# Optimization experiments

Hardware: AMD Instinct MI355X
Metric: run time of the kernel (lower is better)

## Reference

```python
import jax, jax.numpy as jnp
import numpy as np

N_HEAD = 8
N_QP = 4  # query/key points per head
N_VP = 4  # value points per head
D_SPH = 16  # scalar dims per head
SCALE_SCALAR = D_SPH ** (-0.5)
SCALE_POINT = (4.5 * N_QP) ** (-0.5)
SCALE_TOTAL = 3.0 ** (-0.5)  # scalar + pair bias + point logits


def _euclid(xp, r, t):
    # xp: (b,n,l,p,3), r: (b,l,3,3), t: (b,l,3)  -> row-vector convention: x @ r + t
    return jnp.einsum('bnlpk,blkc->bnlpc', xp, r) + t[:, None, :, None, :]


def _inv_euclid(xp, r, t):
    # (x - t) @ r^T
    return jnp.einsum('bnlpk,blck->bnlpc', xp - t[:, None, :, None, :], r)


def setup_inputs() -> dict:
    key = jax.random.key(0)
    ks = jax.random.split(key, 16)
    b, l, d_res, d_pair = 2, 512, 384, 128
    w = lambda k, shp, fan: jax.random.normal(k, shp, jnp.float32) * (fan ** -0.5)
    return {
        'x': jax.random.normal(ks[0], (b, l, d_res), jnp.float32),
        'e': jax.random.normal(ks[1], (b, l, l, d_pair), jnp.float32),
        'r': jax.random.normal(ks[2], (b, l, 3, 3), jnp.float32),
        't': jax.random.normal(ks[3], (b, l, 3), jnp.float32),
        'Wq_s': w(ks[4], (d_res, N_HEAD * D_SPH), d_res),
        'Wk_s': w(ks[5], (d_res, N_HEAD * D_SPH), d_res),
        'Wv_s': w(ks[6], (d_res, N_HEAD * D_SPH), d_res),
        'Wpb': w(ks[7], (d_pair, N_HEAD), d_pair),
        'Wq_p': w(ks[8], (d_res, N_HEAD * N_QP * 3), d_res),
        'Wk_p': w(ks[9], (d_res, N_HEAD * N_QP * 3), d_res),
        'Wv_p': w(ks[10], (d_res, N_HEAD * N_VP * 3), d_res),
        'gamma': jnp.log(jnp.expm1(jnp.ones((N_HEAD,), jnp.float32))),
        'Wout': w(ks[11], (N_HEAD * D_SPH + N_HEAD * d_pair + N_HEAD * N_VP * 3 + N_HEAD * N_VP, d_res), 1280),
        'bout': jnp.zeros((d_res,), jnp.float32),
    }


def reference(x, e, r, t, Wq_s, Wk_s, Wv_s, Wpb, Wq_p, Wk_p, Wv_p, gamma, Wout, bout):
    b, l, _ = x.shape
    n = N_HEAD

    def split_heads(v):  # (b,l,n*d) -> (b,n,l,d)
        return v.reshape(b, l, n, -1).transpose(0, 2, 1, 3)

    def split_points(v, p):  # (b,l,n*p*3) -> (b,n,l,p,3)
        return v.reshape(b, l, n, p, 3).transpose(0, 2, 1, 3, 4)

    q_s, k_s, v_s = (split_heads(x @ W) for W in (Wq_s, Wk_s, Wv_s))
    q_p = _euclid(split_points(x @ Wq_p, N_QP), r, t)
    k_p = _euclid(split_points(x @ Wk_p, N_QP), r, t)
    v_p = _euclid(split_points(x @ Wv_p, N_VP), r, t)

    logit_scalar = jnp.einsum('bnid,bnjd->bnij', q_s, k_s) * SCALE_SCALAR
    bias_pair = (e @ Wpb).transpose(0, 3, 1, 2)  # (b,n,i,j)
    # pairwise squared point distances, summed over points p and coords c
    diff = q_p[:, :, :, None] - k_p[:, :, None]  # (b,n,i,j,p,3)
    sqdist = (diff ** 2).sum(axis=(-1, -2))      # (b,n,i,j)
    logit_point = -0.5 * SCALE_POINT * gamma[None, :, None, None] * sqdist

    attn = jax.nn.softmax(SCALE_TOTAL * (logit_scalar + bias_pair + logit_point), axis=-1)

    out_scalar = jnp.einsum('bnij,bnjd->bnid', attn, v_s).transpose(0, 2, 1, 3).reshape(b, l, -1)
    out_pair = jnp.einsum('bnij,bijd->bnid', attn, e).transpose(0, 2, 1, 3).reshape(b, l, -1)
    out_point = jnp.einsum('bnij,bnjpc->bnipc', attn, v_p)
    out_point = _inv_euclid(out_point, r, t)  # (b,n,i,p,3)
    out_point_norm = jnp.sqrt((out_point ** 2).sum(-1))  # (b,n,i,p)
    out_point = out_point.transpose(0, 2, 1, 3, 4).reshape(b, l, -1)
    out_point_norm = out_point_norm.transpose(0, 2, 1, 3).reshape(b, l, -1)

    out = jnp.concatenate([out_scalar, out_pair, out_point, out_point_norm], axis=-1)
    return out @ Wout + bout
```

## Files before the change

### kernel.cpp

```cpp
#include <hip/hip_runtime.h>
#include <hip/hip_bf16.h>
#include <math.h>

#define NH 8
#define L 512
#define DP 128
#define DS 16
#define DCAT 1280
#define TJ 32
#define NCHUNK 4
#define CJ 128
#define PSTRIDE 1280

#define SCALE_SCALAR 0.25f
#define SCALE_POINT  0.23570226039551584f
#define SCALE_TOTAL  0.5773502691896258f

typedef __bf16 bf16_t;
typedef bf16_t bf16x8 __attribute__((ext_vector_type(8)));
typedef float  f32x4v __attribute__((ext_vector_type(4)));

__global__ __launch_bounds__(256) void k_pack(
    const float* __restrict__ x,
    const float* __restrict__ Wq_s, const float* __restrict__ Wk_s, const float* __restrict__ Wv_s,
    const float* __restrict__ Wq_p, const float* __restrict__ Wk_p, const float* __restrict__ Wv_p,
    __hip_bfloat16* __restrict__ xb, __hip_bfloat16* __restrict__ WallT) {
    int idx = blockIdx.x * 256 + threadIdx.x;
    const int T1 = 1024 * 384;
    if (idx < T1) {
        xb[idx] = __float2bfloat16(x[idx]);
    } else {
        int j = idx - T1;
        int n = j / 384, k = j % 384;
        float v;
        if      (n < 128) v = Wq_s[k * 128 + n];
        else if (n < 256) v = Wk_s[k * 128 + (n - 128)];
        else if (n < 384) v = Wv_s[k * 128 + (n - 256)];
        else if (n < 480) v = Wq_p[k * 96  + (n - 384)];
        else if (n < 576) v = Wk_p[k * 96  + (n - 480)];
        else              v = Wv_p[k * 96  + (n - 576)];
        WallT[(size_t)n * 384 + k] = __float2bfloat16(v);
    }
}

__global__ __launch_bounds__(256) void k_prep(const float* __restrict__ Wout,
                                              __hip_bfloat16* __restrict__ WoutT) {
    __shared__ float tile[64][65];
    const int tid = threadIdx.x;
    const int k0 = blockIdx.x * 64;
    const int n0 = blockIdx.y * 64;
#pragma unroll
    for (int s = 0; s < 16; ++s) {
        int idx = s * 256 + tid, kk = idx >> 6, nn = idx & 63;
        tile[kk][nn] = Wout[(size_t)(k0 + kk) * 384 + n0 + nn];
    }
    __syncthreads();
#pragma unroll
    for (int s = 0; s < 16; ++s) {
        int idx = s * 256 + tid, nn = idx >> 6, kk = idx & 63;
        WoutT[(size_t)(n0 + nn) * 1280 + k0 + kk] = __float2bfloat16(tile[kk][nn]);
    }
}

__global__ __launch_bounds__(256) void k_projm(
    const __hip_bfloat16* __restrict__ xb, const __hip_bfloat16* __restrict__ WallT,
    float* __restrict__ q_s, float* __restrict__ k_s, float* __restrict__ v_s,
    float* __restrict__ praw) {
    __shared__ __align__(16) bf16_t As[64 * 40];
    __shared__ __align__(16) bf16_t Bs[48 * 40];
    const int tid = threadIdx.x;
    const int row0 = blockIdx.x * 64, col0 = blockIdx.y * 48;
    const int w = tid >> 6, lane = tid & 63;
    f32x4v acc[3] = {};

    for (int k0 = 0; k0 < 384; k0 += 32) {
        __syncthreads();
        {
            int rr = tid >> 2, q = tid & 3;
            *reinterpret_cast<int4*>(&As[rr * 40 + q * 8]) =
                *reinterpret_cast<const int4*>(&xb[(size_t)(row0 + rr) * 384 + k0 + q * 8]);
            if (tid < 192)
                *reinterpret_cast<int4*>(&Bs[rr * 40 + q * 8]) =
                    *reinterpret_cast<const int4*>(&WallT[(size_t)(col0 + rr) * 384 + k0 + q * 8]);
        }
        __syncthreads();
        const int m = lane & 15, kq = lane >> 4;
        bf16x8 af = *reinterpret_cast<const bf16x8*>(&As[(w * 16 + m) * 40 + kq * 8]);
#pragma unroll
        for (int c = 0; c < 3; ++c) {
            bf16x8 bfr = *reinterpret_cast<const bf16x8*>(&Bs[(c * 16 + m) * 40 + kq * 8]);
            acc[c] = __builtin_amdgcn_mfma_f32_16x16x32_bf16(af, bfr, acc[c], 0, 0, 0);
        }
    }
    const int colL = lane & 15, rbase = (lane >> 4) * 4;
#pragma unroll
    for (int c = 0; c < 3; ++c) {
        int col = col0 + c * 16 + colL;
#pragma unroll
        for (int rg = 0; rg < 4; ++rg) {
            int row = row0 + w * 16 + rbase + rg;
            float v = acc[c][rg];
            int bb = row >> 9, ll = row & 511;
            if (col < 384) {
                int kind = col >> 7, n = (col >> 4) & 7, d = col & 15;
                float* dst = (kind == 0) ? q_s : (kind == 1) ? k_s : v_s;
                dst[((size_t)(bb * NH + n) * L + ll) * DS + d] = v;
            } else {
                praw[(size_t)row * 288 + (col - 384)] = v;
            }
        }
    }
}

__global__ __launch_bounds__(256) void k_euclid(
    const float* __restrict__ praw, const float* __restrict__ r, const float* __restrict__ t,
    float* __restrict__ q_p, float* __restrict__ k_p, float* __restrict__ v_p) {
    int idx = blockIdx.x * 256 + threadIdx.x;
    int row = idx / 288, o = idx % 288;
    int arr = o / 96, oo = o % 96;
    int n = oo / 12, pc = oo % 12, p = pc / 3, c = pc % 3;
    const float* base = praw + (size_t)row * 288 + arr * 96 + n * 12 + p * 3;
    float acc = t[row * 3 + c];
#pragma unroll
    for (int k = 0; k < 3; ++k) acc += base[k] * r[row * 9 + k * 3 + c];
    float* dst = (arr == 0) ? q_p : (arr == 1) ? k_p : v_p;
    int bb = row >> 9, ll = row & 511;
    dst[((size_t)(bb * NH + n) * L + ll) * 12 + pc] = acc;
}

__global__ __launch_bounds__(256) void k_attn(
    const float* __restrict__ e, const float* __restrict__ Wpb, const float* __restrict__ gamma,
    const float* __restrict__ q_s, const float* __restrict__ k_s, const float* __restrict__ v_s,
    const float* __restrict__ q_p, const float* __restrict__ k_p, const float* __restrict__ v_p,
    float* __restrict__ part) {
    __shared__ __align__(16) float et[TJ * DP];
    __shared__ __align__(16) float wpbT[NH * DP];
    __shared__ float pt[NH][36];
    __shared__ float ptT[TJ][NH];
    __shared__ __align__(16) float qsl[NH * 16];
    __shared__ __align__(16) float qpl[NH * 12];
    __shared__ float gsh[NH];

    const int tid = threadIdx.x;
    const int blk = blockIdx.x;
    const int bi = blk >> 2, chunk = blk & 3;
    const int b = bi >> 9, i = bi & 511, b8 = b * NH;
    const int nH = tid >> 5, jL = tid & 31;
    const int d4 = tid & 31, jsub = tid >> 5;

    for (int idx = tid; idx < NH * DP; idx += 256)
        wpbT[(idx >> 7) * DP + (idx & 127)] = Wpb[(idx & 127) * NH + (idx >> 7)];
    if (tid < 128) {
        int n = tid >> 4, d = tid & 15;
        qsl[n * 16 + d] = q_s[((size_t)(b8 + n) * L + i) * DS + d];
    } else if (tid < 224) {
        int o = tid - 128, n = o / 12, pc = o % 12;
        qpl[n * 12 + pc] = q_p[((size_t)(b8 + n) * L + i) * 12 + pc];
    } else if (tid < 232) {
        gsh[tid - 224] = gamma[tid - 224];
    }

    const int nS = tid >> 4, dS = tid & 15;
    const int oP = tid - 128;
    const int nP = (oP >= 0 && oP < 96) ? oP / 12 : 0;
    const int pcP = (oP >= 0 && oP < 96) ? oP % 12 : 0;
    const float* vsp = v_s + (((size_t)(b8 + nS) * L + chunk * CJ) << 4) + dS;
    const float* vpp = v_p + ((size_t)(b8 + nP) * L + chunk * CJ) * 12 + pcP;

    float lsum = 0.f;
    float4 accPair[NH];
#pragma unroll
    for (int n = 0; n < NH; ++n) accPair[n] = make_float4(0.f, 0.f, 0.f, 0.f);
    float accS = 0.f, accP = 0.f;

    const float4* esrc4 = reinterpret_cast<const float4*>(
        e + ((size_t)(b * L + i) * L + chunk * CJ) * DP);

    for (int tile = 0; tile < CJ / TJ; ++tile) {
        const int j0 = tile * TJ;
        __syncthreads();
#pragma unroll
        for (int s = 0; s < 4; ++s) {
            int idx = tid + s * 256;
            int j = idx >> 5, g = idx & 31;
            float4 v = esrc4[(size_t)(j0 + j) * 32 + g];
            reinterpret_cast<float4*>(et)[j * 32 + (g ^ j)] = v;
        }
        __syncthreads();
        {
            const int jg = chunk * CJ + j0 + jL;
            const float4* row4 = reinterpret_cast<const float4*>(et) + jL * 32;
            const float4* wr4 = reinterpret_cast<const float4*>(&wpbT[nH * DP]);
            float bsum = 0.f;
#pragma unroll 8
            for (int g = 0; g < 32; ++g) {
                float4 ev = row4[g ^ jL];
                float4 wv4 = wr4[g];
                bsum += ev.x * wv4.x + ev.y * wv4.y + ev.z * wv4.z + ev.w * wv4.w;
            }
            const float4* ksr = reinterpret_cast<const float4*>(k_s + (((size_t)(b8 + nH) * L + jg) << 4));
            const float4* q4 = reinterpret_cast<const float4*>(&qsl[nH * 16]);
            float ssum = 0.f;
#pragma unroll
            for (int g = 0; g < 4; ++g) {
                float4 kv = ksr[g], qv = q4[g];
                ssum += kv.x * qv.x + kv.y * qv.y + kv.z * qv.z + kv.w * qv.w;
            }
            const float4* kpr = reinterpret_cast<const float4*>(k_p + ((size_t)(b8 + nH) * L + jg) * 12);
            const float4* qp4 = reinterpret_cast<const float4*>(&qpl[nH * 12]);
            float sq = 0.f;
#pragma unroll
            for (int g = 0; g < 3; ++g) {
                float4 kv = kpr[g], qv = qp4[g];
                float d0;
                d0 = qv.x - kv.x; sq += d0 * d0;  d0 = qv.y - kv.y; sq += d0 * d0;
                d0 = qv.z - kv.z; sq += d0 * d0;  d0 = qv.w - kv.w; sq += d0 * d0;
            }
            float lg = SCALE_TOTAL * (ssum * SCALE_SCALAR + bsum
                                      - 0.5f * SCALE_POINT * gsh[nH] * sq);
            float pv = __expf(lg);
            lsum += pv;
            pt[nH][jL] = pv;
            ptT[jL][nH] = pv;
        }
        __syncthreads();
        {
            const float4* et4 = reinterpret_cast<const float4*>(et);
#pragma unroll
            for (int s = 0; s < 4; ++s) {
                int j = jsub * 4 + s;
                float4 ev = et4[j * 32 + (d4 ^ j)];
                const float4* pb4 = reinterpret_cast<const float4*>(&ptT[j][0]);
                float4 pA = pb4[0], pB = pb4[1];
#define ACCP(nn, ps) accPair[nn].x += (ps) * ev.x; accPair[nn].y += (ps) * ev.y; \
                     accPair[nn].z += (ps) * ev.z; accPair[nn].w += (ps) * ev.w;
                ACCP(0, pA.x) ACCP(1, pA.y) ACCP(2, pA.z) ACCP(3, pA.w)
                ACCP(4, pB.x) ACCP(5, pB.y) ACCP(6, pB.z) ACCP(7, pB.w)
#undef ACCP
            }
        }
        if (tid < 128) {
            const float* vp = vsp + (size_t)j0 * 16;
#pragma unroll
            for (int q = 0; q < 8; ++q) {
                float4 p4 = *reinterpret_cast<const float4*>(&pt[nS][q * 4]);
                accS += p4.x * vp[(q * 4 + 0) * 16] + p4.y * vp[(q * 4 + 1) * 16]
                      + p4.z * vp[(q * 4 + 2) * 16] + p4.w * vp[(q * 4 + 3) * 16];
            }
        } else if (tid < 224) {
            const float* vp = vpp + (size_t)j0 * 12;
#pragma unroll
            for (int q = 0; q < 8; ++q) {
                float4 p4 = *reinterpret_cast<const float4*>(&pt[nP][q * 4]);
                accP += p4.x * vp[(q * 4 + 0) * 12] + p4.y * vp[(q * 4 + 1) * 12]
                      + p4.z * vp[(q * 4 + 2) * 12] + p4.w * vp[(q * 4 + 3) * 12];
            }
        }
    }

    float* prow = part + (size_t)blk * PSTRIDE;
    lsum += __shfl_xor(lsum, 1);  lsum += __shfl_xor(lsum, 2);
    lsum += __shfl_xor(lsum, 4);  lsum += __shfl_xor(lsum, 8);
    lsum += __shfl_xor(lsum, 16);
    if (jL == 0) prow[1248 + nH] = lsum;
    if (tid < 128) prow[1024 + tid] = accS;
    else if (tid < 224) prow[1152 + (tid - 128)] = accP;

    float4* red4 = reinterpret_cast<float4*>(et);
    __syncthreads();
    if (jsub >= 4) {
#pragma unroll
        for (int n = 0; n < NH; ++n) red4[((jsub - 4) * NH + n) * 32 + d4] = accPair[n];
    }
    __syncthreads();
    if (jsub < 4) {
#pragma unroll
        for (int n = 0; n < NH; ++n) {
            float4 o = red4[(jsub * NH + n) * 32 + d4];
            accPair[n].x += o.x; accPair[n].y += o.y; accPair[n].z += o.z; accPair[n].w += o.w;
        }
    }
    __syncthreads();
    if (jsub == 2 || jsub == 3) {
#pragma unroll
        for (int n = 0; n < NH; ++n) red4[((jsub - 2) * NH + n) * 32 + d4] = accPair[n];
    }
    __syncthreads();
    if (jsub < 2) {
#pragma unroll
        for (int n = 0; n < NH; ++n) {
            float4 o = red4[(jsub * NH + n) * 32 + d4];
            accPair[n].x += o.x; accPair[n].y += o.y; accPair[n].z += o.z; accPair[n].w += o.w;
        }
    }
    __syncthreads();
    if (jsub == 1) {
#pragma unroll
        for (int n = 0; n < NH; ++n) red4[n * 32 + d4] = accPair[n];
    }
    __syncthreads();
    if (jsub == 0) {
#pragma unroll
        for (int n = 0; n < NH; ++n) {
            float4 o = red4[n * 32 + d4];
            accPair[n].x += o.x; accPair[n].y += o.y; accPair[n].z += o.z; accPair[n].w += o.w;
            *reinterpret_cast<float4*>(&prow[n * 128 + d4 * 4]) = accPair[n];
        }
    }
}

__global__ __launch_bounds__(256) void k_comb(
    const float* __restrict__ part, const float* __restrict__ r, const float* __restrict__ t,
    __hip_bfloat16* __restrict__ concat) {
    __shared__ float comb[1256];
    __shared__ float rtsh[12], osh[96], o2sh[96];
    const int tid = threadIdx.x;
    const int bi = blockIdx.x;
    const float* base = part + (size_t)bi * NCHUNK * PSTRIDE;
#pragma unroll
    for (int s = 0; s < 5; ++s) {
        int idx = tid + s * 256;
        if (idx < 1256)
            comb[idx] = base[idx] + base[PSTRIDE + idx] + base[2 * PSTRIDE + idx] + base[3 * PSTRIDE + idx];
    }
    if (tid >= 244 && tid < 256) {
        int c = tid - 244;
        rtsh[c] = (c < 9) ? r[bi * 9 + c] : t[bi * 3 + (c - 9)];
    }
    __syncthreads();
    __hip_bfloat16* crow = concat + (size_t)bi * DCAT;
    if (tid < 128) crow[tid] = __float2bfloat16(comb[1024 + tid] / comb[1248 + (tid >> 4)]);
    for (int idx = tid; idx < 1024; idx += 256)
        crow[128 + idx] = __float2bfloat16(comb[idx] / comb[1248 + (idx >> 7)]);
    if (tid >= 128 && tid < 224) {
        int o = tid - 128;
        osh[o] = comb[1152 + o] / comb[1248 + o / 12];
    }
    __syncthreads();
    if (tid < 96) {
        int n = tid / 12, pc = tid % 12, p = pc / 3, c = pc % 3;
        float oc = 0.f;
#pragma unroll
        for (int k = 0; k < 3; ++k)
            oc += (osh[n * 12 + p * 3 + k] - rtsh[9 + k]) * rtsh[c * 3 + k];
        crow[1152 + tid] = __float2bfloat16(oc);
        o2sh[tid] = oc;
    }
    __syncthreads();
    if (tid < 32) {
        int n = tid >> 2, p = tid & 3;
        float vx = o2sh[n * 12 + p * 3], vy = o2sh[n * 12 + p * 3 + 1], vz = o2sh[n * 12 + p * 3 + 2];
        crow[1248 + tid] = __float2bfloat16(sqrtf(vx * vx + vy * vy + vz * vz));
    }
}

__global__ __launch_bounds__(256) void k_out(const __hip_bfloat16* __restrict__ A,
                                             const __hip_bfloat16* __restrict__ Bt,
                                             const float* __restrict__ bout,
                                             float* __restrict__ out) {
    __shared__ __align__(16) bf16_t At[64 * 40];
    __shared__ __align__(16) bf16_t Bs[64 * 40];
    const int tid = threadIdx.x;
    const int row0 = blockIdx.x * 64, col0 = blockIdx.y * 64;
    const int wv = tid >> 6, lane = tid & 63;
    f32x4v acc[4] = {};

    for (int k0 = 0; k0 < 1280; k0 += 32) {
        __syncthreads();
        {
            int rr = tid >> 2, q = tid & 3;
            *reinterpret_cast<int4*>(&At[rr * 40 + q * 8]) =
                *reinterpret_cast<const int4*>(&A[(size_t)(row0 + rr) * 1280 + k0 + q * 8]);
            *reinterpret_cast<int4*>(&Bs[rr * 40 + q * 8]) =
                *reinterpret_cast<const int4*>(&Bt[(size_t)(col0 + rr) * 1280 + k0 + q * 8]);
        }
        __syncthreads();
        const int m = lane & 15, kq = lane >> 4;
        bf16x8 af = *reinterpret_cast<const bf16x8*>(&At[(wv * 16 + m) * 40 + kq * 8]);
#pragma unroll
        for (int nt = 0; nt < 4; ++nt) {
            bf16x8 bfr = *reinterpret_cast<const bf16x8*>(&Bs[(nt * 16 + m) * 40 + kq * 8]);
            acc[nt] = __builtin_amdgcn_mfma_f32_16x16x32_bf16(af, bfr, acc[nt], 0, 0, 0);
        }
    }
    const int col_l = lane & 15, rbase = (lane >> 4) * 4;
#pragma unroll
    for (int nt = 0; nt < 4; ++nt) {
        int col = col0 + nt * 16 + col_l;
        float bo = bout[col];
#pragma unroll
        for (int rg = 0; rg < 4; ++rg) {
            int rowg = row0 + wv * 16 + rbase + rg;
            out[(size_t)rowg * 384 + col] = acc[nt][rg] + bo;
        }
    }
}

extern "C" void kernel_launch(void* const* d_in, const int* in_sizes, int n_in,
                              void* d_out, int out_size, void* d_ws, size_t ws_size,
                              hipStream_t stream) {
    const float* x     = (const float*)d_in[0];
    const float* e     = (const float*)d_in[1];
    const float* r     = (const float*)d_in[2];
    const float* t     = (const float*)d_in[3];
    const float* Wq_s  = (const float*)d_in[4];
    const float* Wk_s  = (const float*)d_in[5];
    const float* Wv_s  = (const float*)d_in[6];
    const float* Wpb   = (const float*)d_in[7];
    const float* Wq_p  = (const float*)d_in[8];
    const float* Wk_p  = (const float*)d_in[9];
    const float* Wv_p  = (const float*)d_in[10];
    const float* gamma = (const float*)d_in[11];
    const float* Wout  = (const float*)d_in[12];
    const float* bout  = (const float*)d_in[13];

    float* ws   = (float*)d_ws;
    float* q_s  = ws + 0;
    float* k_s  = ws + 131072;
    float* v_s  = ws + 262144;
    float* q_p  = ws + 393216;
    float* k_p  = ws + 491520;
    float* v_p  = ws + 589824;
    float* praw = ws + 688128;
    __hip_bfloat16* xb     = (__hip_bfloat16*)((char*)d_ws + 3932160);
    __hip_bfloat16* WallT  = (__hip_bfloat16*)((char*)d_ws + 4718592);
    __hip_bfloat16* concat = (__hip_bfloat16*)((char*)d_ws + 5234688);
    __hip_bfloat16* WoutT  = (__hip_bfloat16*)((char*)d_ws + 7856128);
    float* part = (float*)((char*)d_ws + 8847360);
    float* out = (float*)d_out;

    hipLaunchKernelGGL(k_pack, dim3(2544), dim3(256), 0, stream,
                       x, Wq_s, Wk_s, Wv_s, Wq_p, Wk_p, Wv_p, xb, WallT);
    hipLaunchKernelGGL(k_prep, dim3(20, 6), dim3(256), 0, stream, Wout, WoutT);
    hipLaunchKernelGGL(k_projm, dim3(16, 14), dim3(256), 0, stream,
                       xb, WallT, q_s, k_s, v_s, praw);
    hipLaunchKernelGGL(k_euclid, dim3(1152), dim3(256), 0, stream,
                       praw, r, t, q_p, k_p, v_p);
    hipLaunchKernelGGL(k_attn, dim3(4096), dim3(256), 0, stream,
                       e, Wpb, gamma, q_s, k_s, v_s, q_p, k_p, v_p, part);
    hipLaunchKernelGGL(k_comb, dim3(1024), dim3(256), 0, stream,
                       part, r, t, concat);
    hipLaunchKernelGGL(k_out, dim3(16, 6), dim3(256), 0, stream, concat, WoutT, bout, out);
}
```

Before: 486.6 us.

## Double-buffer pair tiles via direct global-to-LDS loads and split pair-bias reduction

```diff
diff --git a/kernel.cpp b/kernel.cpp
--- a/kernel.cpp
+++ b/kernel.cpp
@@ -133,8 +133,9 @@
     const float* __restrict__ q_s, const float* __restrict__ k_s, const float* __restrict__ v_s,
     const float* __restrict__ q_p, const float* __restrict__ k_p, const float* __restrict__ v_p,
     float* __restrict__ part) {
-    __shared__ __align__(16) float et[TJ * DP];
-    __shared__ __align__(16) float wpbT[NH * DP];
+    __shared__ __align__(16) float et[2][TJ * DP];
+    __shared__ __align__(16) float wpbK[DP * NH];
+    __shared__ float ps[8 * TJ * NH];
     __shared__ float pt[NH][36];
     __shared__ float ptT[TJ][NH];
     __shared__ __align__(16) float qsl[NH * 16];
@@ -148,8 +149,7 @@
     const int nH = tid >> 5, jL = tid & 31;
     const int d4 = tid & 31, jsub = tid >> 5;
 
-    for (int idx = tid; idx < NH * DP; idx += 256)
-        wpbT[(idx >> 7) * DP + (idx & 127)] = Wpb[(idx & 127) * NH + (idx >> 7)];
+    reinterpret_cast<float4*>(wpbK)[tid] = reinterpret_cast<const float4*>(Wpb)[tid];
     if (tid < 128) {
         int n = tid >> 4, d = tid & 15;
         qsl[n * 16 + d] = q_s[((size_t)(b8 + n) * L + i) * DS + d];
@@ -167,40 +167,56 @@
     const float* vsp = v_s + (((size_t)(b8 + nS) * L + chunk * CJ) << 4) + dS;
     const float* vpp = v_p + ((size_t)(b8 + nP) * L + chunk * CJ) * 12 + pcP;
 
-    float lsum = 0.f;
-    float4 accPair[NH];
-#pragma unroll
-    for (int n = 0; n < NH; ++n) accPair[n] = make_float4(0.f, 0.f, 0.f, 0.f);
-    float accS = 0.f, accP = 0.f;
-
     const float4* esrc4 = reinterpret_cast<const float4*>(
         e + ((size_t)(b * L + i) * L + chunk * CJ) * DP);
 
+    const int wbase = tid & 192;
+    auto stage = [&](int buf, int j0) {
+        float* etb = &et[buf][0];
+#pragma unroll
+        for (int s = 0; s < 4; ++s) {
+            int idx = s * 256 + tid;
+            int j = idx >> 5, g = (idx & 31) ^ j;
+            const float* src = reinterpret_cast<const float*>(esrc4 + (size_t)(j0 + j) * 32 + g);
+            __builtin_amdgcn_global_load_lds(
+                (const __attribute__((address_space(1))) void*)src,
+                (__attribute__((address_space(3))) void*)(etb + (size_t)(s * 256 + wbase) * 4),
+                16, 0, 0);
+        }
+    };
+
+    float lsum = 0.f;
+    f32x4v accPair[NH] = {};
+    float accS = 0.f, accP = 0.f;
+
+    stage(0, 0);
+    __syncthreads();
+
+    int cur = 0;
     for (int tile = 0; tile < CJ / TJ; ++tile) {
         const int j0 = tile * TJ;
-        __syncthreads();
-#pragma unroll
-        for (int s = 0; s < 4; ++s) {
-            int idx = tid + s * 256;
-            int j = idx >> 5, g = idx & 31;
-            float4 v = esrc4[(size_t)(j0 + j) * 32 + g];
-            reinterpret_cast<float4*>(et)[j * 32 + (g ^ j)] = v;
-        }
-        __syncthreads();
-        {
-            const int jg = chunk * CJ + j0 + jL;
-            const float4* row4 = reinterpret_cast<const float4*>(et) + jL * 32;
-            const float4* wr4 = reinterpret_cast<const float4*>(&wpbT[nH * DP]);
-            float bsum = 0.f;
-#pragma unroll 8
-            for (int g = 0; g < 32; ++g) {
-                float4 ev = row4[g ^ jL];
-                float4 wv4 = wr4[g];
-                bsum += ev.x * wv4.x + ev.y * wv4.y + ev.z * wv4.z + ev.w * wv4.w;
-            }
+        if (tile < CJ / TJ - 1) stage(cur ^ 1, j0 + TJ);
+
+        const f32x4v* e4 = reinterpret_cast<const f32x4v*>(&et[cur][0]);
+
+        f32x4v a0 = {}, a1 = {};
+        {
+            const f32x4v* wp4 = reinterpret_cast<const f32x4v*>(wpbK);
+#pragma unroll
+            for (int f = 0; f < 4; ++f) {
+                f32x4v ev = e4[jL * 32 + ((nH * 4 + f) ^ jL)];
+                const f32x4v* wk = wp4 + (size_t)(nH * 16 + f * 4) * 2;
+                a0 += ev.x * wk[0]; a1 += ev.x * wk[1];
+                a0 += ev.y * wk[2]; a1 += ev.y * wk[3];
+                a0 += ev.z * wk[4]; a1 += ev.z * wk[5];
+                a0 += ev.w * wk[6]; a1 += ev.w * wk[7];
+            }
+        }
+        const int jg = chunk * CJ + j0 + jL;
+        float ssum = 0.f, sq = 0.f;
+        {
             const float4* ksr = reinterpret_cast<const float4*>(k_s + (((size_t)(b8 + nH) * L + jg) << 4));
             const float4* q4 = reinterpret_cast<const float4*>(&qsl[nH * 16]);
-            float ssum = 0.f;
 #pragma unroll
             for (int g = 0; g < 4; ++g) {
                 float4 kv = ksr[g], qv = q4[g];
@@ -208,7 +224,6 @@
             }
             const float4* kpr = reinterpret_cast<const float4*>(k_p + ((size_t)(b8 + nH) * L + jg) * 12);
             const float4* qp4 = reinterpret_cast<const float4*>(&qpl[nH * 12]);
-            float sq = 0.f;
 #pragma unroll
             for (int g = 0; g < 3; ++g) {
                 float4 kv = kpr[g], qv = qp4[g];
@@ -216,6 +231,21 @@
                 d0 = qv.x - kv.x; sq += d0 * d0;  d0 = qv.y - kv.y; sq += d0 * d0;
                 d0 = qv.z - kv.z; sq += d0 * d0;  d0 = qv.w - kv.w; sq += d0 * d0;
             }
+        }
+        {
+            int pb = (nH * TJ + jL) * NH, sw = jL & 7;
+            ps[pb + (0 ^ sw)] = a0.x; ps[pb + (1 ^ sw)] = a0.y;
+            ps[pb + (2 ^ sw)] = a0.z; ps[pb + (3 ^ sw)] = a0.w;
+            ps[pb + (4 ^ sw)] = a1.x; ps[pb + (5 ^ sw)] = a1.y;
+            ps[pb + (6 ^ sw)] = a1.z; ps[pb + (7 ^ sw)] = a1.w;
+        }
+        __syncthreads();
+
+        {
+            float bsum = 0.f;
+            const int sw = nH ^ (jL & 7);
+#pragma unroll
+            for (int kq = 0; kq < 8; ++kq) bsum += ps[(kq * TJ + jL) * NH + sw];
             float lg = SCALE_TOTAL * (ssum * SCALE_SCALAR + bsum
                                       - 0.5f * SCALE_POINT * gsh[nH] * sq);
             float pv = __expf(lg);
@@ -224,19 +254,18 @@
             ptT[jL][nH] = pv;
         }
         __syncthreads();
-        {
-            const float4* et4 = reinterpret_cast<const float4*>(et);
+
+        {
 #pragma unroll
             for (int s = 0; s < 4; ++s) {
                 int j = jsub * 4 + s;
-                float4 ev = et4[j * 32 + (d4 ^ j)];
+                f32x4v ev = e4[j * 32 + (d4 ^ j)];
                 const float4* pb4 = reinterpret_cast<const float4*>(&ptT[j][0]);
                 float4 pA = pb4[0], pB = pb4[1];
-#define ACCP(nn, ps) accPair[nn].x += (ps) * ev.x; accPair[nn].y += (ps) * ev.y; \
-                     accPair[nn].z += (ps) * ev.z; accPair[nn].w += (ps) * ev.w;
-                ACCP(0, pA.x) ACCP(1, pA.y) ACCP(2, pA.z) ACCP(3, pA.w)
-                ACCP(4, pB.x) ACCP(5, pB.y) ACCP(6, pB.z) ACCP(7, pB.w)
-#undef ACCP
+                accPair[0] += pA.x * ev; accPair[1] += pA.y * ev;
+                accPair[2] += pA.z * ev; accPair[3] += pA.w * ev;
+                accPair[4] += pB.x * ev; accPair[5] += pB.y * ev;
+                accPair[6] += pB.z * ev; accPair[7] += pB.w * ev;
             }
         }
         if (tid < 128) {
@@ -256,6 +285,8 @@
                       + p4.z * vp[(q * 4 + 2) * 12] + p4.w * vp[(q * 4 + 3) * 12];
             }
         }
+        __syncthreads();
+        cur ^= 1;
     }
 
     float* prow = part + (size_t)blk * PSTRIDE;
@@ -266,7 +297,7 @@
     if (tid < 128) prow[1024 + tid] = accS;
     else if (tid < 224) prow[1152 + (tid - 128)] = accP;
 
-    float4* red4 = reinterpret_cast<float4*>(et);
+    f32x4v* red4 = reinterpret_cast<f32x4v*>(&et[0][0]);
     __syncthreads();
     if (jsub >= 4) {
 #pragma unroll
@@ -275,36 +306,29 @@
     __syncthreads();
     if (jsub < 4) {
 #pragma unroll
+        for (int n = 0; n < NH; ++n) accPair[n] += red4[(jsub * NH + n) * 32 + d4];
+    }
+    __syncthreads();
+    if (jsub == 2 || jsub == 3) {
+#pragma unroll
+        for (int n = 0; n < NH; ++n) red4[((jsub - 2) * NH + n) * 32 + d4] = accPair[n];
+    }
+    __syncthreads();
+    if (jsub < 2) {
+#pragma unroll
+        for (int n = 0; n < NH; ++n) accPair[n] += red4[(jsub * NH + n) * 32 + d4];
+    }
+    __syncthreads();
+    if (jsub == 1) {
+#pragma unroll
+        for (int n = 0; n < NH; ++n) red4[n * 32 + d4] = accPair[n];
+    }
+    __syncthreads();
+    if (jsub == 0) {
+#pragma unroll
         for (int n = 0; n < NH; ++n) {
-            float4 o = red4[(jsub * NH + n) * 32 + d4];
-            accPair[n].x += o.x; accPair[n].y += o.y; accPair[n].z += o.z; accPair[n].w += o.w;
-        }
-    }
-    __syncthreads();
-    if (jsub == 2 || jsub == 3) {
-#pragma unroll
-        for (int n = 0; n < NH; ++n) red4[((jsub - 2) * NH + n) * 32 + d4] = accPair[n];
-    }
-    __syncthreads();
-    if (jsub < 2) {
-#pragma unroll
-        for (int n = 0; n < NH; ++n) {
-            float4 o = red4[(jsub * NH + n) * 32 + d4];
-            accPair[n].x += o.x; accPair[n].y += o.y; accPair[n].z += o.z; accPair[n].w += o.w;
-        }
-    }
-    __syncthreads();
-    if (jsub == 1) {
-#pragma unroll
-        for (int n = 0; n < NH; ++n) red4[n * 32 + d4] = accPair[n];
-    }
-    __syncthreads();
-    if (jsub == 0) {
-#pragma unroll
-        for (int n = 0; n < NH; ++n) {
-            float4 o = red4[n * 32 + d4];
-            accPair[n].x += o.x; accPair[n].y += o.y; accPair[n].z += o.z; accPair[n].w += o.w;
-            *reinterpret_cast<float4*>(&prow[n * 128 + d4 * 4]) = accPair[n];
+            accPair[n] += red4[n * 32 + d4];
+            *reinterpret_cast<f32x4v*>(&prow[n * 128 + d4 * 4]) = accPair[n];
         }
     }
 }
```

New measurement: 554.4 us. +13.9%, slower.

## Keep e tile in registers, pad LDS rows, remap bias threads to head-major

Applied to the files above, without the earlier changes.

```diff
diff --git a/kernel.cpp b/kernel.cpp
--- a/kernel.cpp
+++ b/kernel.cpp
@@ -133,23 +133,27 @@
     const float* __restrict__ q_s, const float* __restrict__ k_s, const float* __restrict__ v_s,
     const float* __restrict__ q_p, const float* __restrict__ k_p, const float* __restrict__ v_p,
     float* __restrict__ part) {
-    __shared__ __align__(16) float et[TJ * DP];
-    __shared__ __align__(16) float wpbT[NH * DP];
-    __shared__ float pt[NH][36];
-    __shared__ float ptT[TJ][NH];
+    __shared__ __align__(16) float et[TJ * 132];
+    __shared__ __align__(16) float wpbT[NH * 132];
+    __shared__ __align__(16) float pt[NH][36];
     __shared__ __align__(16) float qsl[NH * 16];
     __shared__ __align__(16) float qpl[NH * 12];
     __shared__ float gsh[NH];
+    __shared__ float lred[32];
 
     const int tid = threadIdx.x;
     const int blk = blockIdx.x;
     const int bi = blk >> 2, chunk = blk & 3;
     const int b = bi >> 9, i = bi & 511, b8 = b * NH;
-    const int nH = tid >> 5, jL = tid & 31;
-    const int d4 = tid & 31, jsub = tid >> 5;
-
-    for (int idx = tid; idx < NH * DP; idx += 256)
-        wpbT[(idx >> 7) * DP + (idx & 127)] = Wpb[(idx & 127) * NH + (idx >> 7)];
+
+    const int wA = tid >> 6, nA = (tid >> 3) & 7, jrA = tid & 7;
+    const int jA = wA * 8 + jrA;
+    const int jr2 = tid >> 5, g = tid & 31;
+
+    for (int idx = tid; idx < NH * DP; idx += 256) {
+        int n = idx >> 7, k = idx & 127;
+        wpbT[n * 132 + k] = Wpb[k * NH + n];
+    }
     if (tid < 128) {
         int n = tid >> 4, d = tid & 15;
         qsl[n * 16 + d] = q_s[((size_t)(b8 + n) * L + i) * DS + d];
@@ -167,76 +171,66 @@
     const float* vsp = v_s + (((size_t)(b8 + nS) * L + chunk * CJ) << 4) + dS;
     const float* vpp = v_p + ((size_t)(b8 + nP) * L + chunk * CJ) * 12 + pcP;
 
+    const f32x4v* esrc4 = reinterpret_cast<const f32x4v*>(
+        e + ((size_t)(b * L + i) * L + chunk * CJ) * DP);
+    f32x4v* et4 = reinterpret_cast<f32x4v*>(et);
+
     float lsum = 0.f;
-    float4 accPair[NH];
-#pragma unroll
-    for (int n = 0; n < NH; ++n) accPair[n] = make_float4(0.f, 0.f, 0.f, 0.f);
+    f32x4v accPair[NH] = {};
     float accS = 0.f, accP = 0.f;
-
-    const float4* esrc4 = reinterpret_cast<const float4*>(
-        e + ((size_t)(b * L + i) * L + chunk * CJ) * DP);
+    f32x4v ev[4];
 
     for (int tile = 0; tile < CJ / TJ; ++tile) {
         const int j0 = tile * TJ;
         __syncthreads();
 #pragma unroll
         for (int s = 0; s < 4; ++s) {
-            int idx = tid + s * 256;
-            int j = idx >> 5, g = idx & 31;
-            float4 v = esrc4[(size_t)(j0 + j) * 32 + g];
-            reinterpret_cast<float4*>(et)[j * 32 + (g ^ j)] = v;
+            int j = jr2 + 8 * s;
+            f32x4v v = esrc4[(size_t)(j0 + j) * 32 + g];
+            et4[j * 33 + g] = v;
+            ev[s] = v;
         }
         __syncthreads();
         {
-            const int jg = chunk * CJ + j0 + jL;
-            const float4* row4 = reinterpret_cast<const float4*>(et) + jL * 32;
-            const float4* wr4 = reinterpret_cast<const float4*>(&wpbT[nH * DP]);
-            float bsum = 0.f;
+            const f32x4v* erow = et4 + jA * 33;
+            const f32x4v* wrow = reinterpret_cast<const f32x4v*>(wpbT) + nA * 33;
+            f32x4v b4 = {};
 #pragma unroll 8
-            for (int g = 0; g < 32; ++g) {
-                float4 ev = row4[g ^ jL];
-                float4 wv4 = wr4[g];
-                bsum += ev.x * wv4.x + ev.y * wv4.y + ev.z * wv4.z + ev.w * wv4.w;
+            for (int gg = 0; gg < 32; ++gg) b4 += erow[gg] * wrow[gg];
+            float bsum = b4[0] + b4[1] + b4[2] + b4[3];
+
+            const int jg = chunk * CJ + j0 + jA;
+            const f32x4v* ksr = reinterpret_cast<const f32x4v*>(k_s + (((size_t)(b8 + nA) * L + jg) << 4));
+            const f32x4v* q4 = reinterpret_cast<const f32x4v*>(&qsl[nA * 16]);
+            f32x4v s4 = {};
+#pragma unroll
+            for (int gg = 0; gg < 4; ++gg) s4 += ksr[gg] * q4[gg];
+            float ssum = s4[0] + s4[1] + s4[2] + s4[3];
+
+            const f32x4v* kpr = reinterpret_cast<const f32x4v*>(k_p + ((size_t)(b8 + nA) * L + jg) * 12);
+            const f32x4v* qp4 = reinterpret_cast<const f32x4v*>(&qpl[nA * 12]);
+            f32x4v d4 = {};
+#pragma unroll
+            for (int gg = 0; gg < 3; ++gg) {
+                f32x4v df = qp4[gg] - kpr[gg];
+                d4 += df * df;
             }
-            const float4* ksr = reinterpret_cast<const float4*>(k_s + (((size_t)(b8 + nH) * L + jg) << 4));
-            const float4* q4 = reinterpret_cast<const float4*>(&qsl[nH * 16]);
-            float ssum = 0.f;
-#pragma unroll
-            for (int g = 0; g < 4; ++g) {
-                float4 kv = ksr[g], qv = q4[g];
-                ssum += kv.x * qv.x + kv.y * qv.y + kv.z * qv.z + kv.w * qv.w;
-            }
-            const float4* kpr = reinterpret_cast<const float4*>(k_p + ((size_t)(b8 + nH) * L + jg) * 12);
-            const float4* qp4 = reinterpret_cast<const float4*>(&qpl[nH * 12]);
-            float sq = 0.f;
-#pragma unroll
-            for (int g = 0; g < 3; ++g) {
-                float4 kv = kpr[g], qv = qp4[g];
-                float d0;
-                d0 = qv.x - kv.x; sq += d0 * d0;  d0 = qv.y - kv.y; sq += d0 * d0;
-                d0 = qv.z - kv.z; sq += d0 * d0;  d0 = qv.w - kv.w; sq += d0 * d0;
-            }
+            float sq = d4[0] + d4[1] + d4[2] + d4[3];
+
             float lg = SCALE_TOTAL * (ssum * SCALE_SCALAR + bsum
-                                      - 0.5f * SCALE_POINT * gsh[nH] * sq);
+                                      - 0.5f * SCALE_POINT * gsh[nA] * sq);
             float pv = __expf(lg);
             lsum += pv;
-            pt[nH][jL] = pv;
-            ptT[jL][nH] = pv;
+            pt[nA][jA] = pv;
         }
         __syncthreads();
         {
-            const float4* et4 = reinterpret_cast<const float4*>(et);
 #pragma unroll
             for (int s = 0; s < 4; ++s) {
-                int j = jsub * 4 + s;
-                float4 ev = et4[j * 32 + (d4 ^ j)];
-                const float4* pb4 = reinterpret_cast<const float4*>(&ptT[j][0]);
-                float4 pA = pb4[0], pB = pb4[1];
-#define ACCP(nn, ps) accPair[nn].x += (ps) * ev.x; accPair[nn].y += (ps) * ev.y; \
-                     accPair[nn].z += (ps) * ev.z; accPair[nn].w += (ps) * ev.w;
-                ACCP(0, pA.x) ACCP(1, pA.y) ACCP(2, pA.z) ACCP(3, pA.w)
-                ACCP(4, pB.x) ACCP(5, pB.y) ACCP(6, pB.z) ACCP(7, pB.w)
-#undef ACCP
+                int j = jr2 + 8 * s;
+#pragma unroll
+                for (int n = 0; n < NH; ++n)
+                    accPair[n] += pt[n][j] * ev[s];
             }
         }
         if (tid < 128) {
@@ -259,52 +253,45 @@
     }
 
     float* prow = part + (size_t)blk * PSTRIDE;
-    lsum += __shfl_xor(lsum, 1);  lsum += __shfl_xor(lsum, 2);
-    lsum += __shfl_xor(lsum, 4);  lsum += __shfl_xor(lsum, 8);
-    lsum += __shfl_xor(lsum, 16);
-    if (jL == 0) prow[1248 + nH] = lsum;
+    lsum += __shfl_xor(lsum, 1);  lsum += __shfl_xor(lsum, 2);  lsum += __shfl_xor(lsum, 4);
+    if (jrA == 0) lred[wA * 8 + nA] = lsum;
     if (tid < 128) prow[1024 + tid] = accS;
     else if (tid < 224) prow[1152 + (tid - 128)] = accP;
-
-    float4* red4 = reinterpret_cast<float4*>(et);
-    __syncthreads();
+    __syncthreads();
+    if (tid < 8) prow[1248 + tid] = lred[tid] + lred[8 + tid] + lred[16 + tid] + lred[24 + tid];
+
+    f32x4v* red4 = reinterpret_cast<f32x4v*>(et);
+    const int d4i = tid & 31, jsub = tid >> 5;
     if (jsub >= 4) {
 #pragma unroll
-        for (int n = 0; n < NH; ++n) red4[((jsub - 4) * NH + n) * 32 + d4] = accPair[n];
+        for (int n = 0; n < NH; ++n) red4[((jsub - 4) * NH + n) * 32 + d4i] = accPair[n];
     }
     __syncthreads();
     if (jsub < 4) {
 #pragma unroll
+        for (int n = 0; n < NH; ++n) accPair[n] += red4[(jsub * NH + n) * 32 + d4i];
+    }
+    __syncthreads();
+    if (jsub == 2 || jsub == 3) {
+#pragma unroll
+        for (int n = 0; n < NH; ++n) red4[((jsub - 2) * NH + n) * 32 + d4i] = accPair[n];
+    }
+    __syncthreads();
+    if (jsub < 2) {
+#pragma unroll
+        for (int n = 0; n < NH; ++n) accPair[n] += red4[(jsub * NH + n) * 32 + d4i];
+    }
+    __syncthreads();
+    if (jsub == 1) {
+#pragma unroll
+        for (int n = 0; n < NH; ++n) red4[n * 32 + d4i] = accPair[n];
+    }
+    __syncthreads();
+    if (jsub == 0) {
+#pragma unroll
         for (int n = 0; n < NH; ++n) {
-            float4 o = red4[(jsub * NH + n) * 32 + d4];
-            accPair[n].x += o.x; accPair[n].y += o.y; accPair[n].z += o.z; accPair[n].w += o.w;
-        }
-    }
-    __syncthreads();
-    if (jsub == 2 || jsub == 3) {
-#pragma unroll
-        for (int n = 0; n < NH; ++n) red4[((jsub - 2) * NH + n) * 32 + d4] = accPair[n];
-    }
-    __syncthreads();
-    if (jsub < 2) {
-#pragma unroll
-        for (int n = 0; n < NH; ++n) {
-            float4 o = red4[(jsub * NH + n) * 32 + d4];
-            accPair[n].x += o.x; accPair[n].y += o.y; accPair[n].z += o.z; accPair[n].w += o.w;
-        }
-    }
-    __syncthreads();
-    if (jsub == 1) {
-#pragma unroll
-        for (int n = 0; n < NH; ++n) red4[n * 32 + d4] = accPair[n];
-    }
-    __syncthreads();
-    if (jsub == 0) {
-#pragma unroll
-        for (int n = 0; n < NH; ++n) {
-            float4 o = red4[n * 32 + d4];
-            accPair[n].x += o.x; accPair[n].y += o.y; accPair[n].z += o.z; accPair[n].w += o.w;
-            *reinterpret_cast<float4*>(&prow[n * 128 + d4 * 4]) = accPair[n];
+            accPair[n] += red4[n * 32 + d4i];
+            *reinterpret_cast<f32x4v*>(&prow[n * 128 + d4i * 4]) = accPair[n];
         }
     }
 }
```

After: 479.8 us. No clear change (-1.4%).
